# Optimization experiments

Measured on AMD Instinct MI355X. Metric: run time of the kernel, lower is better.

## Reference

```python
import jax, jax.numpy as jnp
import numpy as np

B, S, D = 2, 2048, 1024   # batch, seq, hidden_dim
I = 512                   # intermediate_dim (per-expert FFN width)
E = 16                    # num_experts
TOP_K = 2


def setup_inputs() -> dict:
    key = jax.random.key(0)
    ks = jax.random.split(key, 10)
    sc_d = 1.0 / np.sqrt(D)
    sc_i = 1.0 / np.sqrt(I)
    return {
        "x": jax.random.normal(ks[0], (B, S, D), dtype=jnp.float32),
        # router gate: Linear(D -> E) with bias (nnx.Linear default)
        "gate_w": jax.random.normal(ks[1], (D, E), dtype=jnp.float32) * sc_d,
        "gate_b": jnp.zeros((E,), dtype=jnp.float32),
        # shared expert MLP (SwiGLU: down(silu(gate(x)) * up(x)))
        "shared_wg": jax.random.normal(ks[2], (D, I), dtype=jnp.float32) * sc_d,
        "shared_wu": jax.random.normal(ks[3], (D, I), dtype=jnp.float32) * sc_d,
        "shared_wd": jax.random.normal(ks[4], (I, D), dtype=jnp.float32) * sc_i,
        # routed experts, stacked on leading E axis
        "experts_wg": jax.random.normal(ks[5], (E, D, I), dtype=jnp.float32) * sc_d,
        "experts_wu": jax.random.normal(ks[6], (E, D, I), dtype=jnp.float32) * sc_d,
        "experts_wd": jax.random.normal(ks[7], (E, I, D), dtype=jnp.float32) * sc_i,
    }


def _mlp(x, wg, wu, wd):
    # SwiGLU MLP: down(silu(gate(x)) * up(x))
    return jnp.einsum("bsi,id->bsd", jax.nn.silu(x @ wg) * (x @ wu), wd)


def reference(x, gate_w, gate_b, shared_wg, shared_wu, shared_wd,
              experts_wg, experts_wu, experts_wd):
    # router: sigmoid logits -> top_k -> normalize by sum of selected scores
    router_logits = jax.nn.sigmoid(x @ gate_w + gate_b)          # [B,S,E]
    expert_values, expert_indices = jax.lax.top_k(router_logits, k=TOP_K)
    expert_values = expert_values / jnp.sum(expert_values, axis=-1, keepdims=True)

    # dense all-expert compute (faithful to source): [B,S,E,D]
    hg = jnp.einsum("bsd,edi->bsei", x, experts_wg)
    hu = jnp.einsum("bsd,edi->bsei", x, experts_wu)
    all_outputs = jnp.einsum("bsei,eid->bsed", jax.nn.silu(hg) * hu, experts_wd)

    # gather top-k expert outputs: [B,S,K,D]
    selected = jnp.take_along_axis(all_outputs, expert_indices[..., None], axis=2)
    expert_weighted = jnp.sum(expert_values[..., None] * selected, axis=2)  # [B,S,D]

    return x + _mlp(x, shared_wg, shared_wu, shared_wd) + expert_weighted
```

## Files before the change

kernel.cpp:

```cpp
#include <hip/hip_runtime.h>
#include <stdint.h>

typedef __attribute__((ext_vector_type(8))) short short8;
typedef __attribute__((ext_vector_type(4))) float f32x4;

#define TOKENS 4096
#define DDIM 1024
#define IDIM 512
#define NEXP 16
#define NEXP1 17
#define CSTRIDE 32
#define MAXMB 112

#define OFF_WGU   0ull
#define OFF_WD    35651584ull
#define OFF_XB    53477376ull
#define OFF_HGU   61865984ull
#define OFF_H     87031808ull
#define OFF_TOK   99614720ull
#define OFF_REC   99893248ull
#define OFF_WREC  99926016ull
#define OFF_CNT   100171776ull
#define OFF_BASE  100175872ull

#define TICKET_IDX 768

__device__ __forceinline__ float bf2f(unsigned short u) {
    union { uint32_t i; float f; } v; v.i = ((uint32_t)u) << 16; return v.f;
}
__device__ __forceinline__ unsigned short f2bf(float f) {
    union { float f; uint32_t i; } v; v.f = f;
    uint32_t r = v.i + 0x7FFFu + ((v.i >> 16) & 1u);
    return (unsigned short)(r >> 16);
}
__device__ __forceinline__ void cp16(const unsigned short* g, unsigned short* l) {
    __builtin_amdgcn_global_load_lds(
        (const __attribute__((address_space(1))) uint32_t*)g,
        (__attribute__((address_space(3))) uint32_t*)l, 16, 0, 0);
}

__global__ __launch_bounds__(256)
void k_transpose(const float* __restrict__ eg, const float* __restrict__ eu,
                 const float* __restrict__ ed, const float* __restrict__ sg,
                 const float* __restrict__ su, const float* __restrict__ sd,
                 unsigned short* __restrict__ Wgu, unsigned short* __restrict__ Wd)
{
    int z = blockIdx.z;
    int e = z / 3, m = z % 3;
    int R = (m == 2) ? 512 : 1024;
    int C = (m == 2) ? 1024 : 512;
    int r0 = blockIdx.y * 64, c0 = blockIdx.x * 64;
    if (r0 >= R || c0 >= C) return;
    const float* src;
    if (m == 0)      src = (e < 16) ? eg + (size_t)e * 524288 : sg;
    else if (m == 1) src = (e < 16) ? eu + (size_t)e * 524288 : su;
    else             src = (e < 16) ? ed + (size_t)e * 524288 : sd;

    __shared__ float tl[64 * 65];
    const int tid = threadIdx.x;

    {
        const int lr = tid >> 4;
        const int lc = (tid & 15) * 4;
        #pragma unroll
        for (int ps = 0; ps < 4; ++ps) {
            int r = ps * 16 + lr;
            float4 v = *(const float4*)(src + (size_t)(r0 + r) * C + (c0 + lc));
            float* d = &tl[r * 65 + lc];
            d[0] = v.x; d[1] = v.y; d[2] = v.z; d[3] = v.w;
        }
    }
    __syncthreads();

    {
        const int w = tid >> 6, l = tid & 63;
        const int kb = (l & 7) * 8;
        #pragma unroll
        for (int p = 0; p < 2; ++p) {
            int nl = p * 32 + w * 8 + (l >> 3);
            unsigned short ov[8];
            #pragma unroll
            for (int j = 0; j < 8; ++j)
                ov[j] = f2bf(tl[(kb + j) * 65 + nl]);
            int n = c0 + nl;
            int k = r0 + kb;
            unsigned short* dst;
            if (m < 2) dst = Wgu + (size_t)e * 1048576 + (size_t)(2 * n + m) * 1024 + k;
            else       dst = Wd  + (size_t)e * 524288  + (size_t)n * 512 + k;
            *(uint4*)dst = *(uint4*)ov;
        }
    }
}

__global__ __launch_bounds__(512, 3)
void k_route(const float* __restrict__ x, const float* __restrict__ gw,
             const float* __restrict__ gb, unsigned short* __restrict__ xb,
             int* __restrict__ tok, int2* __restrict__ rec,
             float2* __restrict__ wrec, int* __restrict__ counts,
             int* __restrict__ bases, int* __restrict__ mbp)
{
    __shared__ float gws[1024 * 13];

    const int bid = blockIdx.x;
    const int tid = threadIdx.x;

    {
        const int b0 = bid * 2048;
        #pragma unroll
        for (int c = 0; c < 4; ++c) {
            int i = b0 + c * 512 + tid;
            float4 v = ((const float4*)x)[i];
            ushort4 b;
            b.x = f2bf(v.x); b.y = f2bf(v.y); b.z = f2bf(v.z); b.w = f2bf(v.w);
            ((ushort4*)xb)[i] = b;
        }
        if (tid < 8) tok[16 * 4096 + bid * 8 + tid] = bid * 8 + tid;
    }

    const int t = bid * 8 + (tid >> 6);
    const int lane = tid & 63;
    const float* xr = x + (size_t)t * DDIM;

    float xv[16];
    #pragma unroll
    for (int kk = 0; kk < 16; ++kk) xv[kk] = xr[kk * 64 + lane];

    float v[16];

    for (int p = 0; p < 2; ++p) {
        __syncthreads();
        #pragma unroll
        for (int c = 0; c < 4; ++c) {
            int idx = tid + c * 512;
            int k = idx >> 1;
            int h = (idx & 1) * 4;
            float4 g4 = *(const float4*)(gw + k * 16 + p * 8 + h);
            *(float4*)&gws[k * 13 + h] = g4;
        }
        __syncthreads();

        double a[8];
        #pragma unroll
        for (int j = 0; j < 8; ++j) a[j] = 0.0;

        #pragma unroll
        for (int kk = 0; kk < 16; ++kk) {
            int kl = kk * 64 + lane;
            float4 gA = *(const float4*)&gws[kl * 13];
            float4 gB = *(const float4*)&gws[kl * 13 + 4];
            double xd = (double)xv[kk];
            a[0] += xd * (double)gA.x; a[1] += xd * (double)gA.y;
            a[2] += xd * (double)gA.z; a[3] += xd * (double)gA.w;
            a[4] += xd * (double)gB.x; a[5] += xd * (double)gB.y;
            a[6] += xd * (double)gB.z; a[7] += xd * (double)gB.w;
        }

        #pragma unroll
        for (int off = 32; off > 0; off >>= 1) {
            #pragma unroll
            for (int j = 0; j < 8; ++j)
                a[j] += __shfl_xor(a[j], off, 64);
        }

        #pragma unroll
        for (int j = 0; j < 8; ++j)
            v[p * 8 + j] = 1.0f / (1.0f + expf(-(float)(a[j] + (double)gb[p * 8 + j])));
    }

    if (lane == 0) {
        int i0 = 0;
        #pragma unroll
        for (int e = 1; e < 16; ++e) if (v[e] > v[i0]) i0 = e;
        int i1 = (i0 == 0) ? 1 : 0;
        #pragma unroll
        for (int e = 0; e < 16; ++e) if (e != i0 && e != i1 && v[e] > v[i1]) i1 = e;
        float s = v[i0] + v[i1];
        float w0 = v[i0] / s, w1 = v[i1] / s;
        int p0 = atomicAdd(&counts[i0 * CSTRIDE], 1);
        tok[i0 * 4096 + p0] = t;
        int p1 = atomicAdd(&counts[i1 * CSTRIDE], 1);
        tok[i1 * 4096 + p1] = t;
        rec[t]  = make_int2(i0 * 4096 + p0, i1 * 4096 + p1);
        wrec[t] = make_float2(w0, w1);
    }

    __syncthreads();
    if (tid == 0) {
        __threadfence();
        if (atomicAdd(&counts[TICKET_IDX], 1) == (int)gridDim.x - 1) {
            counts[16 * CSTRIDE] = TOKENS;
            int a = 0, b = 0;
            for (int e = 0; e < NEXP1; ++e) {
                int c = (e < 16) ? atomicAdd(&counts[e * CSTRIDE], 0) : TOKENS;
                bases[e] = a; a += c;
                mbp[e] = b;  b += (c + 127) >> 7;
            }
            bases[17] = a;
            mbp[17] = b;
        }
    }
}

template <int MODE>
__global__ __launch_bounds__(256, 3)
void k_gemm(const unsigned short* __restrict__ Amat, const unsigned short* __restrict__ Bmat,
            const int* __restrict__ tok, const int* __restrict__ counts,
            const int* __restrict__ bases, const int* __restrict__ mbp,
            unsigned short* __restrict__ Out)
{
    constexpr int K = (MODE == 0) ? 1024 : 512;
    const int my = blockIdx.y;
    if (my >= mbp[17]) return;
    int e = 0;
    while (my >= mbp[e + 1]) ++e;
    const int cnt = counts[e * CSTRIDE];
    const int m0 = (my - mbp[e]) * 128;
    const int n0 = blockIdx.x * 128;
    const int base = bases[e];

    __shared__ unsigned short As0[128 * 32];
    __shared__ unsigned short As1[128 * 32];
    __shared__ unsigned short Bs0[128 * 32];
    __shared__ unsigned short Bs1[128 * 32];

    const int tid  = threadIdx.x;
    const int wave = tid >> 6;
    const int lane = tid & 63;
    const int lrow = lane >> 2;
    const int lseg = lane & 3;

    unsigned short* a0d0 = &As0[wave * 1024];
    unsigned short* a0d1 = &As0[wave * 1024 + 512];
    unsigned short* a1d0 = &As1[wave * 1024];
    unsigned short* a1d1 = &As1[wave * 1024 + 512];
    unsigned short* b0d0 = &Bs0[wave * 1024];
    unsigned short* b0d1 = &Bs0[wave * 1024 + 512];
    unsigned short* b1d0 = &Bs1[wave * 1024];
    unsigned short* b1d1 = &Bs1[wave * 1024 + 512];

    int ar0 = m0 + wave * 32 + lrow;      if (ar0 > cnt - 1) ar0 = cnt - 1;
    int ar1 = m0 + wave * 32 + 16 + lrow; if (ar1 > cnt - 1) ar1 = cnt - 1;
    size_t ai0, ai1;
    if (MODE == 0) { ai0 = (size_t)tok[e * 4096 + ar0]; ai1 = (size_t)tok[e * 4096 + ar1]; }
    else           { ai0 = (size_t)(base + ar0);        ai1 = (size_t)(base + ar1); }
    const unsigned short* ag0 = Amat + ai0 * K + lseg * 8;
    const unsigned short* ag1 = Amat + ai1 * K + lseg * 8;
    const size_t eoff = (size_t)e * 1024 * K;
    const unsigned short* bg0 = Bmat + eoff + (size_t)(n0 + wave * 32 + lrow) * K + lseg * 8;
    const unsigned short* bg1 = Bmat + eoff + (size_t)(n0 + wave * 32 + 16 + lrow) * K + lseg * 8;

    const int wm = wave & 1, wn = wave >> 1;
    const int q = lane >> 4, mc = lane & 15;

    f32x4 acc[4][4];
    #pragma unroll
    for (int i = 0; i < 4; ++i)
        #pragma unroll
        for (int j = 0; j < 4; ++j) acc[i][j] = (f32x4){0.f, 0.f, 0.f, 0.f};

    for (int k0 = 0; k0 < K; k0 += 64) {
        __syncthreads();
        cp16(ag0 + k0,      a0d0);
        cp16(ag0 + k0 + 32, a1d0);
        cp16(ag1 + k0,      a0d1);
        cp16(ag1 + k0 + 32, a1d1);
        cp16(bg0 + k0,      b0d0);
        cp16(bg0 + k0 + 32, b1d0);
        cp16(bg1 + k0,      b0d1);
        cp16(bg1 + k0 + 32, b1d1);
        __syncthreads();
        short8 a0[4], b0[4], a1[4], b1[4];
        #pragma unroll
        for (int i = 0; i < 4; ++i) {
            a0[i] = *(const short8*)&As0[(wm * 64 + i * 16 + mc) * 32 + q * 8];
            a1[i] = *(const short8*)&As1[(wm * 64 + i * 16 + mc) * 32 + q * 8];
        }
        #pragma unroll
        for (int j = 0; j < 4; ++j) {
            b0[j] = *(const short8*)&Bs0[(wn * 64 + j * 16 + mc) * 32 + q * 8];
            b1[j] = *(const short8*)&Bs1[(wn * 64 + j * 16 + mc) * 32 + q * 8];
        }
        #pragma unroll
        for (int i = 0; i < 4; ++i)
            #pragma unroll
            for (int j = 0; j < 4; ++j)
                acc[i][j] = __builtin_amdgcn_mfma_f32_16x16x32_bf16(a0[i], b0[j], acc[i][j], 0, 0, 0);
        #pragma unroll
        for (int i = 0; i < 4; ++i)
            #pragma unroll
            for (int j = 0; j < 4; ++j)
                acc[i][j] = __builtin_amdgcn_mfma_f32_16x16x32_bf16(a1[i], b1[j], acc[i][j], 0, 0, 0);
    }

    #pragma unroll
    for (int i = 0; i < 4; ++i) {
        int lr = wm * 64 + i * 16 + q * 4;
        #pragma unroll
        for (int r = 0; r < 4; ++r) {
            int mrow = m0 + lr + r;
            if (mrow >= cnt) continue;
            #pragma unroll
            for (int j = 0; j < 4; ++j) {
                int gc = n0 + wn * 64 + j * 16 + mc;
                float val = acc[i][j][r];
                if (MODE == 0) {
                    float other = __shfl_xor(val, 1, 64);
                    float g = (mc & 1) ? other : val;
                    float u = (mc & 1) ? val : other;
                    float h = g / (1.0f + __expf(-g)) * u;
                    if ((mc & 1) == 0)
                        Out[(size_t)(base + mrow) * 512 + (gc >> 1)] = f2bf(h);
                } else {
                    Out[(size_t)(base + mrow) * 1024 + gc] = f2bf(val);
                }
            }
        }
    }
}

__global__ void k_combine(const float* __restrict__ x, const unsigned short* __restrict__ Hs,
                          const int2* __restrict__ rec, const float2* __restrict__ wrec,
                          const int* __restrict__ bases, float* __restrict__ out)
{
    int t = blockIdx.x * 2 + (threadIdx.x >> 7);
    int c = (threadIdx.x & 127) * 8;
    int2 r = rec[t];
    float2 w = wrec[t];
    int s0 = bases[r.x >> 12] + (r.x & 4095);
    int s1 = bases[r.y >> 12] + (r.y & 4095);
    int ss = 8192 + t;

    unsigned short h0[8], h1[8], hs[8];
    *(uint4*)h0 = *(const uint4*)(Hs + (size_t)s0 * 1024 + c);
    *(uint4*)h1 = *(const uint4*)(Hs + (size_t)s1 * 1024 + c);
    *(uint4*)hs = *(const uint4*)(Hs + (size_t)ss * 1024 + c);
    const float* xr = x + (size_t)t * 1024 + c;
    float o[8];
    #pragma unroll
    for (int j = 0; j < 8; ++j)
        o[j] = xr[j] + bf2f(hs[j]) + w.x * bf2f(h0[j]) + w.y * bf2f(h1[j]);
    float* orow = out + (size_t)t * 1024 + c;
    *(float4*)orow       = *(float4*)&o[0];
    *(float4*)(orow + 4) = *(float4*)&o[4];
}

extern "C" void kernel_launch(void* const* d_in, const int* in_sizes, int n_in,
                              void* d_out, int out_size, void* d_ws, size_t ws_size,
                              hipStream_t stream)
{
    const float* x  = (const float*)d_in[0];
    const float* gw = (const float*)d_in[1];
    const float* gb = (const float*)d_in[2];
    const float* sg = (const float*)d_in[3];
    const float* su = (const float*)d_in[4];
    const float* sd = (const float*)d_in[5];
    const float* eg = (const float*)d_in[6];
    const float* eu = (const float*)d_in[7];
    const float* ed = (const float*)d_in[8];
    float* out = (float*)d_out;
    char* ws = (char*)d_ws;

    unsigned short* Wgu = (unsigned short*)(ws + OFF_WGU);
    unsigned short* Wd  = (unsigned short*)(ws + OFF_WD);
    unsigned short* xb  = (unsigned short*)(ws + OFF_XB);
    unsigned short* Hgu = (unsigned short*)(ws + OFF_HGU);
    unsigned short* H   = (unsigned short*)(ws + OFF_H);
    int*    tok   = (int*)(ws + OFF_TOK);
    int2*   rec   = (int2*)(ws + OFF_REC);
    float2* wrec  = (float2*)(ws + OFF_WREC);
    int*    counts= (int*)(ws + OFF_CNT);
    int*    bases = (int*)(ws + OFF_BASE);
    int*    mbp   = bases + 20;

    (void)hipMemsetAsync(counts, 0, 4096, stream);
    k_transpose<<<dim3(16, 16, 51), 256, 0, stream>>>(eg, eu, ed, sg, su, sd, Wgu, Wd);
    k_route<<<512, 512, 0, stream>>>(x, gw, gb, xb, tok, rec, wrec, counts, bases, mbp);
    k_gemm<0><<<dim3(8, MAXMB), 256, 0, stream>>>(xb, Wgu, tok, counts, bases, mbp, H);
    k_gemm<1><<<dim3(8, MAXMB), 256, 0, stream>>>(H, Wd, tok, counts, bases, mbp, Hgu);
    k_combine<<<2048, 256, 0, stream>>>(x, Hgu, rec, wrec, bases, out);
}
```

Before: 291.3 us.

## Precompute GEMM tile table, remap workgroups per XCD, swizzle LDS reads

The router's last block now builds a per-M-block table holding expert, row offset, base and count, so GEMM blocks read one int4 instead of scanning prefix arrays. The GEMM grid becomes 1D with a workgroup remap that groups consecutive tiles onto the same XCD to improve L2 reuse. A XOR swizzle is also applied to the LDS load segments and the matching MFMA fragment reads to reduce bank conflicts. The risks are that the swizzle must match the global_load_lds lane-to-address mapping exactly, and that the table adds a little serial work to the router's final block.

Result: no change. 287.6 us (-1.3%).

```diff
diff --git a/kernel.cpp b/kernel.cpp
--- a/kernel.cpp
+++ b/kernel.cpp
@@ -20,6 +20,7 @@
 #define OFF_TOK   99614720ull
 #define OFF_REC   99893248ull
 #define OFF_WREC  99926016ull
+#define OFF_MYTAB 99958784ull
 #define OFF_CNT   100171776ull
 #define OFF_BASE  100175872ull
 
@@ -97,9 +98,11 @@
              const float* __restrict__ gb, unsigned short* __restrict__ xb,
              int* __restrict__ tok, int2* __restrict__ rec,
              float2* __restrict__ wrec, int* __restrict__ counts,
-             int* __restrict__ bases, int* __restrict__ mbp)
+             int* __restrict__ bases, int4* __restrict__ mytab)
 {
     __shared__ float gws[1024 * 13];
+    __shared__ int pfx[40];
+    __shared__ int winflag;
 
     const int bid = blockIdx.x;
     const int tid = threadIdx.x;
@@ -187,16 +190,34 @@
     __syncthreads();
     if (tid == 0) {
         __threadfence();
-        if (atomicAdd(&counts[TICKET_IDX], 1) == (int)gridDim.x - 1) {
-            counts[16 * CSTRIDE] = TOKENS;
+        winflag = (atomicAdd(&counts[TICKET_IDX], 1) == (int)gridDim.x - 1) ? 1 : 0;
+    }
+    __syncthreads();
+    if (winflag) {
+        if (tid == 0) {
             int a = 0, b = 0;
-            for (int e = 0; e < NEXP1; ++e) {
-                int c = (e < 16) ? atomicAdd(&counts[e * CSTRIDE], 0) : TOKENS;
-                bases[e] = a; a += c;
-                mbp[e] = b;  b += (c + 127) >> 7;
+            for (int e2 = 0; e2 < NEXP1; ++e2) {
+                int c = (e2 < 16) ? atomicAdd(&counts[e2 * CSTRIDE], 0) : TOKENS;
+                pfx[e2] = a; pfx[20 + e2] = b;
+                bases[e2] = a;
+                a += c; b += (c + 127) >> 7;
             }
+            pfx[17] = a; pfx[37] = b;
             bases[17] = a;
-            mbp[17] = b;
+        }
+        __syncthreads();
+        const int nmb = pfx[37];
+        for (int idx = tid; idx < MAXMB; idx += 512) {
+            int4 val = make_int4(0, 0, 0, 0);
+            if (idx < nmb) {
+                int e2 = 0;
+                #pragma unroll
+                for (int i2 = 1; i2 <= 16; ++i2)
+                    if (idx >= pfx[20 + i2]) e2 = i2;
+                val = make_int4(e2, (idx - pfx[20 + e2]) * 128,
+                                pfx[e2], pfx[e2 + 1] - pfx[e2]);
+            }
+            mytab[idx] = val;
         }
     }
 }
@@ -204,19 +225,17 @@
 template <int MODE>
 __global__ __launch_bounds__(256, 3)
 void k_gemm(const unsigned short* __restrict__ Amat, const unsigned short* __restrict__ Bmat,
-            const int* __restrict__ tok, const int* __restrict__ counts,
-            const int* __restrict__ bases, const int* __restrict__ mbp,
+            const int* __restrict__ tok, const int4* __restrict__ mytab,
             unsigned short* __restrict__ Out)
 {
     constexpr int K = (MODE == 0) ? 1024 : 512;
-    const int my = blockIdx.y;
-    if (my >= mbp[17]) return;
-    int e = 0;
-    while (my >= mbp[e + 1]) ++e;
-    const int cnt = counts[e * CSTRIDE];
-    const int m0 = (my - mbp[e]) * 128;
-    const int n0 = blockIdx.x * 128;
-    const int base = bases[e];
+    const int lin = blockIdx.x;
+    const int wg  = (lin & 7) * MAXMB + (lin >> 3);
+    const int my  = wg >> 3;
+    const int n0  = (wg & 7) * 128;
+    const int4 tt = mytab[my];
+    const int e = tt.x, m0 = tt.y, base = tt.z, cnt = tt.w;
+    if (m0 >= cnt) return;
 
     __shared__ unsigned short As0[128 * 32];
     __shared__ unsigned short As1[128 * 32];
@@ -227,7 +246,7 @@
     const int wave = tid >> 6;
     const int lane = tid & 63;
     const int lrow = lane >> 2;
-    const int lseg = lane & 3;
+    const int lseg = (lane & 3) ^ ((lrow >> 1) & 3);
 
     unsigned short* a0d0 = &As0[wave * 1024];
     unsigned short* a0d1 = &As0[wave * 1024 + 512];
@@ -251,6 +270,7 @@
 
     const int wm = wave & 1, wn = wave >> 1;
     const int q = lane >> 4, mc = lane & 15;
+    const int qs = (q ^ ((mc >> 1) & 3)) * 8;
 
     f32x4 acc[4][4];
     #pragma unroll
@@ -272,13 +292,13 @@
         short8 a0[4], b0[4], a1[4], b1[4];
         #pragma unroll
         for (int i = 0; i < 4; ++i) {
-            a0[i] = *(const short8*)&As0[(wm * 64 + i * 16 + mc) * 32 + q * 8];
-            a1[i] = *(const short8*)&As1[(wm * 64 + i * 16 + mc) * 32 + q * 8];
+            a0[i] = *(const short8*)&As0[(wm * 64 + i * 16 + mc) * 32 + qs];
+            a1[i] = *(const short8*)&As1[(wm * 64 + i * 16 + mc) * 32 + qs];
         }
         #pragma unroll
         for (int j = 0; j < 4; ++j) {
-            b0[j] = *(const short8*)&Bs0[(wn * 64 + j * 16 + mc) * 32 + q * 8];
-            b1[j] = *(const short8*)&Bs1[(wn * 64 + j * 16 + mc) * 32 + q * 8];
+            b0[j] = *(const short8*)&Bs0[(wn * 64 + j * 16 + mc) * 32 + qs];
+            b1[j] = *(const short8*)&Bs1[(wn * 64 + j * 16 + mc) * 32 + qs];
         }
         #pragma unroll
         for (int i = 0; i < 4; ++i)
@@ -368,14 +388,14 @@
     int*    tok   = (int*)(ws + OFF_TOK);
     int2*   rec   = (int2*)(ws + OFF_REC);
     float2* wrec  = (float2*)(ws + OFF_WREC);
+    int4*   mytab = (int4*)(ws + OFF_MYTAB);
     int*    counts= (int*)(ws + OFF_CNT);
     int*    bases = (int*)(ws + OFF_BASE);
-    int*    mbp   = bases + 20;
 
     (void)hipMemsetAsync(counts, 0, 4096, stream);
     k_transpose<<<dim3(16, 16, 51), 256, 0, stream>>>(eg, eu, ed, sg, su, sd, Wgu, Wd);
-    k_route<<<512, 512, 0, stream>>>(x, gw, gb, xb, tok, rec, wrec, counts, bases, mbp);
-    k_gemm<0><<<dim3(8, MAXMB), 256, 0, stream>>>(xb, Wgu, tok, counts, bases, mbp, H);
-    k_gemm<1><<<dim3(8, MAXMB), 256, 0, stream>>>(H, Wd, tok, counts, bases, mbp, Hgu);
+    k_route<<<512, 512, 0, stream>>>(x, gw, gb, xb, tok, rec, wrec, counts, bases, mytab);
+    k_gemm<0><<<8 * MAXMB, 256, 0, stream>>>(xb, Wgu, tok, mytab, H);
+    k_gemm<1><<<8 * MAXMB, 256, 0, stream>>>(H, Wd, tok, mytab, Hgu);
     k_combine<<<2048, 256, 0, stream>>>(x, Hgu, rec, wrec, bases, out);
 }
```
